# Kernel tuning notes

Hardware: AMD Instinct MI355X
Metric: run time of the kernel (lower is better)

Reference implementation:

```python
import jax, jax.numpy as jnp
import numpy as np

N_NODES = 10000
N_EDGES = 160000
NEG_SLOPE = 0.2


def _gat_layer(x, src, dst, W, a_src, a_dst, bias, concat):
    # x: [N, F_in]; W: [F_in, H*C]; a_src/a_dst: [H, C]; bias: [H*C] or [C]
    N = x.shape[0]
    H, C = a_src.shape
    h = (x @ W).reshape(N, H, C)                       # [N,H,C]
    al_s = jnp.einsum('nhc,hc->nh', h, a_src)          # [N,H]
    al_d = jnp.einsum('nhc,hc->nh', h, a_dst)          # [N,H]
    e = jax.nn.leaky_relu(al_s[src] + al_d[dst], NEG_SLOPE)  # [E,H]
    # segment softmax over incoming edges of each destination node
    m = jax.ops.segment_max(e, dst, num_segments=N)    # [N,H]
    ex = jnp.exp(e - m[dst])
    denom = jax.ops.segment_sum(ex, dst, num_segments=N)
    alpha = ex / (denom[dst] + 1e-16)                  # [E,H]
    msg = h[src] * alpha[:, :, None]                   # [E,H,C]
    out = jax.ops.segment_sum(msg, dst, num_segments=N)  # [N,H,C]
    out = out.reshape(N, H * C) if concat else out.mean(axis=1)
    return out + bias


def setup_inputs() -> dict:
    key = jax.random.key(0)
    ks = jax.random.split(key, 10)
    in_dim, hid, out_dim, heads = 768, 512, 768, 4
    x = jax.random.normal(ks[0], (N_NODES, in_dim), dtype=jnp.float32)
    edge_index = jax.random.randint(ks[1], (2, N_EDGES), 0, N_NODES, dtype=jnp.int64)
    g = lambda k, shape, fan: jax.random.normal(k, shape, jnp.float32) / np.sqrt(fan)
    return {
        'x': x,
        'edge_index': edge_index,
        'W1': g(ks[2], (in_dim, heads * hid), in_dim),
        'att_src1': g(ks[3], (heads, hid), hid),
        'att_dst1': g(ks[4], (heads, hid), hid),
        'b1': jnp.zeros((heads * hid,), jnp.float32),
        'W2': g(ks[5], (heads * hid, out_dim), heads * hid),
        'att_src2': g(ks[6], (1, out_dim), out_dim),
        'att_dst2': g(ks[7], (1, out_dim), out_dim),
        'b2': jnp.zeros((out_dim,), jnp.float32),
    }


def reference(x, edge_index, W1, att_src1, att_dst1, b1, W2, att_src2, att_dst2, b2):
    N = x.shape[0]
    loops = jnp.arange(N, dtype=edge_index.dtype)
    src = jnp.concatenate([edge_index[0], loops])  # PyG GATConv adds self-loops
    dst = jnp.concatenate([edge_index[1], loops])
    h = jax.nn.elu(_gat_layer(x, src, dst, W1, att_src1, att_dst1, b1, concat=True))
    out = _gat_layer(h, src, dst, W2, att_src2, att_dst2, b2, concat=False)
    return out
```

## Files before the change

### kernel.cpp

```cpp
#include <hip/hip_runtime.h>
#include <hip/hip_bf16.h>
#include <math.h>

#define N_NODES 10000
#define N_EDGES0 160000
#define E_TOT (N_EDGES0 + N_NODES)
#define H1 4
#define C1 512
#define F1 2048
#define IN_DIM 768
#define C2 768
#define NEG_SLOPE 0.2f

typedef _Float16 f16x8 __attribute__((ext_vector_type(8)));
typedef _Float16 f16x4 __attribute__((ext_vector_type(4)));
typedef float f32x4 __attribute__((ext_vector_type(4)));

typedef __attribute__((address_space(1))) const void* gas_ptr;
typedef __attribute__((address_space(3))) void* las_ptr;
static __device__ __forceinline__ void gload16(const void* g, void* l) {
  __builtin_amdgcn_global_load_lds((gas_ptr)g, (las_ptr)l, 16, 0, 0);
}

static __device__ __forceinline__ unsigned enc_f(float v) {
  unsigned u = __float_as_uint(v);
  return (u & 0x80000000u) ? ~u : (u | 0x80000000u);
}
static __device__ __forceinline__ float dec_f(unsigned u) {
  return (u & 0x80000000u) ? __uint_as_float(u ^ 0x80000000u)
                           : __uint_as_float(~u);
}

static __device__ __forceinline__ void edge_sd(const int* __restrict__ ei, int e,
                                               int& s, int& d) {
  if (e < N_EDGES0) { s = ei[e]; d = ei[N_EDGES0 + e]; }
  else { s = e - N_EDGES0; d = s; }
}

__global__ void split_k(const float* __restrict__ in, _Float16* __restrict__ hi,
                        _Float16* __restrict__ lo, int n4) {
  int i = blockIdx.x * blockDim.x + threadIdx.x;
  if (i >= n4) return;
  float4 v = ((const float4*)in)[i];
  f16x4 h, l;
  h.x = (_Float16)v.x; l.x = (_Float16)(v.x - (float)h.x);
  h.y = (_Float16)v.y; l.y = (_Float16)(v.y - (float)h.y);
  h.z = (_Float16)v.z; l.z = (_Float16)(v.z - (float)h.z);
  h.w = (_Float16)v.w; l.w = (_Float16)(v.w - (float)h.w);
  ((f16x4*)hi)[i] = h;
  ((f16x4*)lo)[i] = l;
}

__global__ void tsplit_k(const float* __restrict__ W, _Float16* __restrict__ hi,
                         _Float16* __restrict__ lo, int K, int N) {
  __shared__ float tile[32][33];
  const int nb = blockIdx.x * 32, kb = blockIdx.y * 32;
  const int tx = threadIdx.x, ty = threadIdx.y;
  for (int r = ty; r < 32; r += 8)
    tile[r][tx] = W[(size_t)(kb + r) * N + nb + tx];
  __syncthreads();
  for (int r = ty; r < 32; r += 8) {
    float v = tile[tx][r];
    _Float16 h = (_Float16)v;
    hi[(size_t)(nb + r) * K + kb + tx] = h;
    lo[(size_t)(nb + r) * K + kb + tx] = (_Float16)(v - (float)h);
  }
}

__global__ __launch_bounds__(256) void gemm_sf16(
    const _Float16* __restrict__ Ahi, const _Float16* __restrict__ Alo,
    const _Float16* __restrict__ Bhi, const _Float16* __restrict__ Blo,
    float* __restrict__ C, int M, int N, int K) {
  __shared__ _Float16 sAh[128 * 32];
  __shared__ _Float16 sAl[128 * 32];
  __shared__ _Float16 sBh[128 * 32];
  __shared__ _Float16 sBl[128 * 32];

  const int t = threadIdx.x;
  const int w = t >> 6, lane = t & 63;
  const int m0 = blockIdx.y * 128, n0 = blockIdx.x * 128;

  const int o0 = w * 1024 + lane * 16;
  const int o1 = o0 + 4096;
  const int ma0 = o0 >> 6, cb0 = o0 & 63;
  const int ma1 = o1 >> 6, cb1 = o1 & 63;
  const int rA0 = min(m0 + ma0, M - 1), rA1 = min(m0 + ma1, M - 1);
  const size_t gA0 = (size_t)rA0 * K + (cb0 >> 1);
  const size_t gA1 = (size_t)rA1 * K + (cb1 >> 1);
  const size_t gB0 = (size_t)(n0 + ma0) * K + (cb0 >> 1);
  const size_t gB1 = (size_t)(n0 + ma1) * K + (cb1 >> 1);

  char* lA0 = (char*)sAh + w * 1024;
  char* lA1 = lA0 + 4096;
  char* lAl0 = (char*)sAl + w * 1024;
  char* lAl1 = lAl0 + 4096;
  char* lB0 = (char*)sBh + w * 1024;
  char* lB1 = lB0 + 4096;
  char* lBl0 = (char*)sBl + w * 1024;
  char* lBl1 = lBl0 + 4096;

  const int wr = w >> 1, wc = w & 1;
  const int lr = lane & 15, lg = lane >> 4;
  const int aoff = (wr * 64 + lr) * 32 + lg * 8;
  const int boff = (wc * 64 + lr) * 32 + lg * 8;

  f32x4 acc[4][4];
#pragma unroll
  for (int i = 0; i < 4; i++)
#pragma unroll
    for (int j = 0; j < 4; j++) acc[i][j] = (f32x4)(0.f);

  for (int k0 = 0; k0 < K; k0 += 32) {
    __syncthreads();
    gload16(Ahi + gA0 + k0, lA0);
    gload16(Ahi + gA1 + k0, lA1);
    gload16(Alo + gA0 + k0, lAl0);
    gload16(Alo + gA1 + k0, lAl1);
    gload16(Bhi + gB0 + k0, lB0);
    gload16(Bhi + gB1 + k0, lB1);
    gload16(Blo + gB0 + k0, lBl0);
    gload16(Blo + gB1 + k0, lBl1);
    __syncthreads();

    f16x8 ah[4], al[4], bh[4], bl[4];
#pragma unroll
    for (int i = 0; i < 4; i++) {
      ah[i] = *(const f16x8*)&sAh[aoff + i * 16 * 32];
      al[i] = *(const f16x8*)&sAl[aoff + i * 16 * 32];
      bh[i] = *(const f16x8*)&sBh[boff + i * 16 * 32];
      bl[i] = *(const f16x8*)&sBl[boff + i * 16 * 32];
    }
#pragma unroll
    for (int i = 0; i < 4; i++)
#pragma unroll
      for (int j = 0; j < 4; j++) {
        acc[i][j] = __builtin_amdgcn_mfma_f32_16x16x32_f16(ah[i], bh[j], acc[i][j], 0, 0, 0);
        acc[i][j] = __builtin_amdgcn_mfma_f32_16x16x32_f16(ah[i], bl[j], acc[i][j], 0, 0, 0);
        acc[i][j] = __builtin_amdgcn_mfma_f32_16x16x32_f16(al[i], bh[j], acc[i][j], 0, 0, 0);
      }
  }

#pragma unroll
  for (int i = 0; i < 4; i++)
#pragma unroll
    for (int j = 0; j < 4; j++) {
      const int col = n0 + wc * 64 + j * 16 + lr;
      const int rbase = m0 + wr * 64 + i * 16 + lg * 4;
#pragma unroll
      for (int r = 0; r < 4; r++) {
        int row = rbase + r;
        if (row < M) C[(size_t)row * N + col] = acc[i][j][r];
      }
    }
}

__global__ void attn_logits(const float* __restrict__ h,
                            const float* __restrict__ asrc,
                            const float* __restrict__ adst,
                            float* __restrict__ als, float* __restrict__ ald,
                            int NH, int Hh, int C) {
  int w = (blockIdx.x * blockDim.x + threadIdx.x) >> 6;
  int lane = threadIdx.x & 63;
  if (w >= NH) return;
  int hh = w % Hh;
  const float* hp = h + (size_t)w * C;
  const float* sp = asrc + hh * C;
  const float* dp = adst + hh * C;
  float ss = 0.f, sd = 0.f;
  for (int c = lane; c < C; c += 64) {
    float v = hp[c];
    ss = fmaf(v, sp[c], ss);
    sd = fmaf(v, dp[c], sd);
  }
#pragma unroll
  for (int o = 32; o; o >>= 1) {
    ss += __shfl_xor(ss, o);
    sd += __shfl_xor(sd, o);
  }
  if (lane == 0) { als[w] = ss; ald[w] = sd; }
}

__global__ void edge_max_k(const int* __restrict__ ei,
                           const float* __restrict__ als,
                           const float* __restrict__ ald,
                           float* __restrict__ ev, unsigned* __restrict__ menc,
                           int Hh) {
  int idx = blockIdx.x * blockDim.x + threadIdx.x;
  if (idx >= E_TOT * Hh) return;
  int e = idx / Hh, hh = idx - e * Hh;
  int s, d; edge_sd(ei, e, s, d);
  float x = als[s * Hh + hh] + ald[d * Hh + hh];
  float v = x > 0.f ? x : NEG_SLOPE * x;
  ev[idx] = v;
  atomicMax(&menc[d * Hh + hh], enc_f(v));
}

__global__ void edge_exp_k(const int* __restrict__ ei,
                           const unsigned* __restrict__ menc,
                           float* __restrict__ ev, float* __restrict__ denom,
                           int Hh) {
  int idx = blockIdx.x * blockDim.x + threadIdx.x;
  if (idx >= E_TOT * Hh) return;
  int e = idx / Hh, hh = idx - e * Hh;
  int s, d; edge_sd(ei, e, s, d);
  float m = dec_f(menc[d * Hh + hh]);
  float ex = expf(ev[idx] - m);
  ev[idx] = ex;
  atomicAdd(&denom[d * Hh + hh], ex);
}

__global__ void hist_k(const int* __restrict__ ei, int* __restrict__ count) {
  int e = blockIdx.x * blockDim.x + threadIdx.x;
  if (e >= E_TOT) return;
  int s, d; edge_sd(ei, e, s, d);
  atomicAdd(&count[d], 1);
}

__global__ __launch_bounds__(1024) void scan_k(const int* __restrict__ count,
                                               int* __restrict__ rowstart,
                                               int N, int total) {
  __shared__ int sums[1024];
  __shared__ int carry_s;
  int t = threadIdx.x;
  if (t == 0) carry_s = 0;
  __syncthreads();
  for (int base = 0; base < N; base += 1024) {
    int i = base + t;
    int c = (i < N) ? count[i] : 0;
    sums[t] = c;
    __syncthreads();
    for (int off = 1; off < 1024; off <<= 1) {
      int v = (t >= off) ? sums[t - off] : 0;
      __syncthreads();
      sums[t] += v;
      __syncthreads();
    }
    int carry = carry_s;
    if (i < N) rowstart[i] = carry + sums[t] - c;
    __syncthreads();
    if (t == 1023) carry_s = carry + sums[1023];
    __syncthreads();
  }
  if (t == 0) rowstart[N] = total;
}

__global__ void scatter_k(const int* __restrict__ ei,
                          const int* __restrict__ rowstart,
                          int* __restrict__ cursor,
                          int* __restrict__ csr_src, int* __restrict__ csr_eid) {
  int e = blockIdx.x * blockDim.x + threadIdx.x;
  if (e >= E_TOT) return;
  int s, d; edge_sd(ei, e, s, d);
  int pos = rowstart[d] + atomicAdd(&cursor[d], 1);
  csr_src[pos] = s;
  csr_eid[pos] = e;
}

template <int FT, bool ELU, bool SPLIT>
__global__ void aggregate_k(const float* __restrict__ hsrc,
                            const float* __restrict__ ev,
                            const float* __restrict__ denom,
                            const float* __restrict__ bias,
                            const int* __restrict__ rowstart,
                            const int* __restrict__ csr_src,
                            const int* __restrict__ csr_eid,
                            float* __restrict__ out,
                            _Float16* __restrict__ ohi, _Float16* __restrict__ olo,
                            int Hh, int C) {
  const int n = blockIdx.x;
  const int t = threadIdx.x;
  const int F = Hh * C;
  const int f0 = t * FT;
  const int hh = f0 / C;
  const float inv = 1.f / (denom[n * Hh + hh] + 1e-16f);
  float acc[FT];
#pragma unroll
  for (int i = 0; i < FT; i++) acc[i] = 0.f;
  const int j0 = rowstart[n], j1 = rowstart[n + 1];
  for (int j = j0; j < j1; j++) {
    int s = csr_src[j];
    int eid = csr_eid[j];
    float wgt = ev[eid * Hh + hh] * inv;
    const float* hp = hsrc + (size_t)s * F + f0;
#pragma unroll
    for (int i = 0; i < FT; i += 4) {
      float4 v = *(const float4*)(hp + i);
      acc[i]     = fmaf(wgt, v.x, acc[i]);
      acc[i + 1] = fmaf(wgt, v.y, acc[i + 1]);
      acc[i + 2] = fmaf(wgt, v.z, acc[i + 2]);
      acc[i + 3] = fmaf(wgt, v.w, acc[i + 3]);
    }
  }
  if (SPLIT) {
    f16x8 h, l;
#pragma unroll
    for (int i = 0; i < FT; i++) {
      float o = acc[i] + bias[f0 + i];
      if (ELU) o = o > 0.f ? o : expm1f(o);
      _Float16 hv = (_Float16)o;
      h[i & 7] = hv;
      l[i & 7] = (_Float16)(o - (float)hv);
    }
    *(f16x8*)&ohi[(size_t)n * F + f0] = h;
    *(f16x8*)&olo[(size_t)n * F + f0] = l;
  } else {
#pragma unroll
    for (int i = 0; i < FT; i++) {
      float o = acc[i] + bias[f0 + i];
      if (ELU) o = o > 0.f ? o : expm1f(o);
      out[(size_t)n * F + f0 + i] = o;
    }
  }
}

extern "C" void kernel_launch(void* const* d_in, const int* in_sizes, int n_in,
                              void* d_out, int out_size, void* d_ws, size_t ws_size,
                              hipStream_t stream) {
  const float* x   = (const float*)d_in[0];
  const int*   ei  = (const int*)d_in[1];
  const float* W1  = (const float*)d_in[2];
  const float* as1 = (const float*)d_in[3];
  const float* ad1 = (const float*)d_in[4];
  const float* b1  = (const float*)d_in[5];
  const float* W2  = (const float*)d_in[6];
  const float* as2 = (const float*)d_in[7];
  const float* ad2 = (const float*)d_in[8];
  const float* b2  = (const float*)d_in[9];
  float* out = (float*)d_out;

  char* p = (char*)d_ws;
  auto alloc = [&](size_t bytes) {
    char* r = p;
    p += (bytes + 255) & ~(size_t)255;
    return r;
  };
  float*     h1    = (float*)alloc((size_t)N_NODES * F1 * 4);
  _Float16*  xhi   = (_Float16*)alloc((size_t)N_NODES * IN_DIM * 2);
  _Float16*  xlo   = (_Float16*)alloc((size_t)N_NODES * IN_DIM * 2);
  _Float16*  W1hi  = (_Float16*)alloc((size_t)IN_DIM * F1 * 2);
  _Float16*  W1lo  = (_Float16*)alloc((size_t)IN_DIM * F1 * 2);
  _Float16*  W2hi  = (_Float16*)alloc((size_t)F1 * C2 * 2);
  _Float16*  W2lo  = (_Float16*)alloc((size_t)F1 * C2 * 2);
  _Float16*  h2hi  = (_Float16*)alloc((size_t)N_NODES * F1 * 2);
  _Float16*  h2lo  = (_Float16*)alloc((size_t)N_NODES * F1 * 2);
  float*     als   = (float*)alloc((size_t)N_NODES * H1 * 4);
  float*     ald   = (float*)alloc((size_t)N_NODES * H1 * 4);
  unsigned*  menc  = (unsigned*)alloc((size_t)N_NODES * H1 * 4);
  float*     denom = (float*)alloc((size_t)N_NODES * H1 * 4);
  float*     ev    = (float*)alloc((size_t)E_TOT * H1 * 4);
  int*       count    = (int*)alloc((size_t)N_NODES * 4);
  int*       rowstart = (int*)alloc((size_t)(N_NODES + 1) * 4);
  int*       cursor   = (int*)alloc((size_t)N_NODES * 4);
  int*       csr_src  = (int*)alloc((size_t)E_TOT * 4);
  int*       csr_eid  = (int*)alloc((size_t)E_TOT * 4);
  float*     h3 = h1;

  const int EB = (E_TOT + 255) / 256;

  hipMemsetAsync(count, 0, (size_t)N_NODES * 4, stream);
  hipMemsetAsync(cursor, 0, (size_t)N_NODES * 4, stream);
  hist_k<<<EB, 256, 0, stream>>>(ei, count);
  scan_k<<<1, 1024, 0, stream>>>(count, rowstart, N_NODES, E_TOT);
  scatter_k<<<EB, 256, 0, stream>>>(ei, rowstart, cursor, csr_src, csr_eid);

  split_k<<<(N_NODES * IN_DIM / 4 + 255) / 256, 256, 0, stream>>>(x, xhi, xlo,
                                                                  N_NODES * IN_DIM / 4);
  tsplit_k<<<dim3(F1 / 32, IN_DIM / 32), dim3(32, 8), 0, stream>>>(W1, W1hi, W1lo,
                                                                   IN_DIM, F1);
  tsplit_k<<<dim3(C2 / 32, F1 / 32), dim3(32, 8), 0, stream>>>(W2, W2hi, W2lo,
                                                               F1, C2);

  gemm_sf16<<<dim3(F1 / 128, (N_NODES + 127) / 128), 256, 0, stream>>>(
      xhi, xlo, W1hi, W1lo, h1, N_NODES, F1, IN_DIM);
  attn_logits<<<(N_NODES * H1) / 4, 256, 0, stream>>>(h1, as1, ad1, als, ald,
                                                      N_NODES * H1, H1, C1);
  hipMemsetAsync(menc, 0, (size_t)N_NODES * H1 * 4, stream);
  hipMemsetAsync(denom, 0, (size_t)N_NODES * H1 * 4, stream);
  edge_max_k<<<(E_TOT * H1 + 255) / 256, 256, 0, stream>>>(ei, als, ald, ev, menc, H1);
  edge_exp_k<<<(E_TOT * H1 + 255) / 256, 256, 0, stream>>>(ei, menc, ev, denom, H1);
  aggregate_k<8, true, true><<<N_NODES, 256, 0, stream>>>(
      h1, ev, denom, b1, rowstart, csr_src, csr_eid, nullptr, h2hi, h2lo, H1, C1);

  gemm_sf16<<<dim3(C2 / 128, (N_NODES + 127) / 128), 256, 0, stream>>>(
      h2hi, h2lo, W2hi, W2lo, h3, N_NODES, C2, F1);
  attn_logits<<<N_NODES / 4, 256, 0, stream>>>(h3, as2, ad2, als, ald,
                                               N_NODES, 1, C2);
  hipMemsetAsync(menc, 0, (size_t)N_NODES * 4, stream);
  hipMemsetAsync(denom, 0, (size_t)N_NODES * 4, stream);
  edge_max_k<<<EB, 256, 0, stream>>>(ei, als, ald, ev, menc, 1);
  edge_exp_k<<<EB, 256, 0, stream>>>(ei, menc, ev, denom, 1);
  aggregate_k<4, false, false><<<N_NODES, 192, 0, stream>>>(
      h3, ev, denom, b2, rowstart, csr_src, csr_eid, out, nullptr, nullptr, 1, C2);
}
```

Measured before the change: 723.0 us.

## Fuse attention logits into GEMM epilogue and store edge weights in CSR order

The attention-logit dot products move into the GEMM epilogue: each wave reduces its accumulator tile against att_src/att_dst with shuffles and atomically adds partial sums per row and head. This removes the separate attn_logits kernel and its re-read of h. Edge exp values are now written in CSR order through a csr_pos map, so aggregation reads them contiguously without the eid indirection. The aggregation loop is unrolled across several edges to keep more gathers in flight, and the softmax normalization is applied once at the end. In exchange, the GEMM epilogue gains atomics and two extra memsets.

```diff
diff --git a/kernel.cpp b/kernel.cpp
--- a/kernel.cpp
+++ b/kernel.cpp
@@ -70,7 +70,9 @@
 __global__ __launch_bounds__(256) void gemm_sf16(
     const _Float16* __restrict__ Ahi, const _Float16* __restrict__ Alo,
     const _Float16* __restrict__ Bhi, const _Float16* __restrict__ Blo,
-    float* __restrict__ C, int M, int N, int K) {
+    float* __restrict__ C, int M, int N, int K,
+    const float* __restrict__ asrc, const float* __restrict__ adst,
+    float* __restrict__ als, float* __restrict__ ald, int Hh, int Cdim) {
   __shared__ _Float16 sAh[128 * 32];
   __shared__ _Float16 sAl[128 * 32];
   __shared__ _Float16 sBh[128 * 32];
@@ -152,32 +154,38 @@
         if (row < M) C[(size_t)row * N + col] = acc[i][j][r];
       }
     }
-}
-
-__global__ void attn_logits(const float* __restrict__ h,
-                            const float* __restrict__ asrc,
-                            const float* __restrict__ adst,
-                            float* __restrict__ als, float* __restrict__ ald,
-                            int NH, int Hh, int C) {
-  int w = (blockIdx.x * blockDim.x + threadIdx.x) >> 6;
-  int lane = threadIdx.x & 63;
-  if (w >= NH) return;
-  int hh = w % Hh;
-  const float* hp = h + (size_t)w * C;
-  const float* sp = asrc + hh * C;
-  const float* dp = adst + hh * C;
-  float ss = 0.f, sd = 0.f;
-  for (int c = lane; c < C; c += 64) {
-    float v = hp[c];
-    ss = fmaf(v, sp[c], ss);
-    sd = fmaf(v, dp[c], sd);
-  }
-#pragma unroll
-  for (int o = 32; o; o >>= 1) {
-    ss += __shfl_xor(ss, o);
-    sd += __shfl_xor(sd, o);
-  }
-  if (lane == 0) { als[w] = ss; ald[w] = sd; }
+
+  const int head = n0 / Cdim;
+  const int cbase = n0 - head * Cdim + wc * 64 + lr;
+  float asv[4], adv[4];
+#pragma unroll
+  for (int j = 0; j < 4; j++) {
+    asv[j] = asrc[(size_t)head * Cdim + cbase + j * 16];
+    adv[j] = adst[(size_t)head * Cdim + cbase + j * 16];
+  }
+#pragma unroll
+  for (int i = 0; i < 4; i++) {
+    const int rbase = m0 + wr * 64 + i * 16 + lg * 4;
+#pragma unroll
+    for (int r = 0; r < 4; r++) {
+      float ss = 0.f, sd = 0.f;
+#pragma unroll
+      for (int j = 0; j < 4; j++) {
+        float v = acc[i][j][r];
+        ss = fmaf(v, asv[j], ss);
+        sd = fmaf(v, adv[j], sd);
+      }
+#pragma unroll
+      for (int o = 8; o; o >>= 1) {
+        ss += __shfl_xor(ss, o);
+        sd += __shfl_xor(sd, o);
+      }
+      if (lr == 0 && rbase + r < M) {
+        atomicAdd(&als[(size_t)(rbase + r) * Hh + head], ss);
+        atomicAdd(&ald[(size_t)(rbase + r) * Hh + head], sd);
+      }
+    }
+  }
 }
 
 __global__ void edge_max_k(const int* __restrict__ ei,
@@ -197,7 +205,9 @@
 
 __global__ void edge_exp_k(const int* __restrict__ ei,
                            const unsigned* __restrict__ menc,
-                           float* __restrict__ ev, float* __restrict__ denom,
+                           const float* __restrict__ ev,
+                           const int* __restrict__ csr_pos,
+                           float* __restrict__ evs, float* __restrict__ denom,
                            int Hh) {
   int idx = blockIdx.x * blockDim.x + threadIdx.x;
   if (idx >= E_TOT * Hh) return;
@@ -205,7 +215,7 @@
   int s, d; edge_sd(ei, e, s, d);
   float m = dec_f(menc[d * Hh + hh]);
   float ex = expf(ev[idx] - m);
-  ev[idx] = ex;
+  evs[(size_t)csr_pos[e] * Hh + hh] = ex;
   atomicAdd(&denom[d * Hh + hh], ex);
 }
 
@@ -247,26 +257,23 @@
 __global__ void scatter_k(const int* __restrict__ ei,
                           const int* __restrict__ rowstart,
                           int* __restrict__ cursor,
-                          int* __restrict__ csr_src, int* __restrict__ csr_eid) {
+                          int* __restrict__ csr_src, int* __restrict__ csr_pos) {
   int e = blockIdx.x * blockDim.x + threadIdx.x;
   if (e >= E_TOT) return;
   int s, d; edge_sd(ei, e, s, d);
   int pos = rowstart[d] + atomicAdd(&cursor[d], 1);
   csr_src[pos] = s;
-  csr_eid[pos] = e;
+  csr_pos[e] = pos;
 }
 
 template <int FT, bool ELU, bool SPLIT>
-__global__ void aggregate_k(const float* __restrict__ hsrc,
-                            const float* __restrict__ ev,
-                            const float* __restrict__ denom,
-                            const float* __restrict__ bias,
-                            const int* __restrict__ rowstart,
-                            const int* __restrict__ csr_src,
-                            const int* __restrict__ csr_eid,
-                            float* __restrict__ out,
-                            _Float16* __restrict__ ohi, _Float16* __restrict__ olo,
-                            int Hh, int C) {
+__global__ __launch_bounds__(256) void aggregate_k(
+    const float* __restrict__ hsrc, const float* __restrict__ evs,
+    const float* __restrict__ denom, const float* __restrict__ bias,
+    const int* __restrict__ rowstart, const int* __restrict__ csr_src,
+    float* __restrict__ out,
+    _Float16* __restrict__ ohi, _Float16* __restrict__ olo,
+    int Hh, int C) {
   const int n = blockIdx.x;
   const int t = threadIdx.x;
   const int F = Hh * C;
@@ -277,25 +284,52 @@
 #pragma unroll
   for (int i = 0; i < FT; i++) acc[i] = 0.f;
   const int j0 = rowstart[n], j1 = rowstart[n + 1];
-  for (int j = j0; j < j1; j++) {
+
+  constexpr int UN = (FT == 8) ? 4 : 8;
+  int j = j0;
+  for (; j + UN <= j1; j += UN) {
+    int   sidx[UN];
+    float wv[UN];
+#pragma unroll
+    for (int u = 0; u < UN; u++) sidx[u] = csr_src[j + u];
+#pragma unroll
+    for (int u = 0; u < UN; u++) wv[u] = evs[(size_t)(j + u) * Hh + hh];
+    float4 va[UN][FT / 4];
+#pragma unroll
+    for (int u = 0; u < UN; u++) {
+      const float* hp = hsrc + (size_t)sidx[u] * F + f0;
+#pragma unroll
+      for (int q = 0; q < FT / 4; q++) va[u][q] = *(const float4*)(hp + q * 4);
+    }
+#pragma unroll
+    for (int u = 0; u < UN; u++)
+#pragma unroll
+      for (int q = 0; q < FT / 4; q++) {
+        acc[q * 4 + 0] = fmaf(wv[u], va[u][q].x, acc[q * 4 + 0]);
+        acc[q * 4 + 1] = fmaf(wv[u], va[u][q].y, acc[q * 4 + 1]);
+        acc[q * 4 + 2] = fmaf(wv[u], va[u][q].z, acc[q * 4 + 2]);
+        acc[q * 4 + 3] = fmaf(wv[u], va[u][q].w, acc[q * 4 + 3]);
+      }
+  }
+  for (; j < j1; j++) {
     int s = csr_src[j];
-    int eid = csr_eid[j];
-    float wgt = ev[eid * Hh + hh] * inv;
+    float wgt = evs[(size_t)j * Hh + hh];
     const float* hp = hsrc + (size_t)s * F + f0;
 #pragma unroll
-    for (int i = 0; i < FT; i += 4) {
-      float4 v = *(const float4*)(hp + i);
-      acc[i]     = fmaf(wgt, v.x, acc[i]);
-      acc[i + 1] = fmaf(wgt, v.y, acc[i + 1]);
-      acc[i + 2] = fmaf(wgt, v.z, acc[i + 2]);
-      acc[i + 3] = fmaf(wgt, v.w, acc[i + 3]);
-    }
-  }
+    for (int q = 0; q < FT / 4; q++) {
+      float4 v = *(const float4*)(hp + q * 4);
+      acc[q * 4 + 0] = fmaf(wgt, v.x, acc[q * 4 + 0]);
+      acc[q * 4 + 1] = fmaf(wgt, v.y, acc[q * 4 + 1]);
+      acc[q * 4 + 2] = fmaf(wgt, v.z, acc[q * 4 + 2]);
+      acc[q * 4 + 3] = fmaf(wgt, v.w, acc[q * 4 + 3]);
+    }
+  }
+
   if (SPLIT) {
     f16x8 h, l;
 #pragma unroll
     for (int i = 0; i < FT; i++) {
-      float o = acc[i] + bias[f0 + i];
+      float o = acc[i] * inv + bias[f0 + i];
       if (ELU) o = o > 0.f ? o : expm1f(o);
       _Float16 hv = (_Float16)o;
       h[i & 7] = hv;
@@ -306,7 +340,7 @@
   } else {
 #pragma unroll
     for (int i = 0; i < FT; i++) {
-      float o = acc[i] + bias[f0 + i];
+      float o = acc[i] * inv + bias[f0 + i];
       if (ELU) o = o > 0.f ? o : expm1f(o);
       out[(size_t)n * F + f0 + i] = o;
     }
@@ -348,11 +382,12 @@
   unsigned*  menc  = (unsigned*)alloc((size_t)N_NODES * H1 * 4);
   float*     denom = (float*)alloc((size_t)N_NODES * H1 * 4);
   float*     ev    = (float*)alloc((size_t)E_TOT * H1 * 4);
+  float*     evs   = (float*)alloc((size_t)E_TOT * H1 * 4);
   int*       count    = (int*)alloc((size_t)N_NODES * 4);
   int*       rowstart = (int*)alloc((size_t)(N_NODES + 1) * 4);
   int*       cursor   = (int*)alloc((size_t)N_NODES * 4);
   int*       csr_src  = (int*)alloc((size_t)E_TOT * 4);
-  int*       csr_eid  = (int*)alloc((size_t)E_TOT * 4);
+  int*       csr_pos  = (int*)alloc((size_t)E_TOT * 4);
   float*     h3 = h1;
 
   const int EB = (E_TOT + 255) / 256;
@@ -361,7 +396,7 @@
   hipMemsetAsync(cursor, 0, (size_t)N_NODES * 4, stream);
   hist_k<<<EB, 256, 0, stream>>>(ei, count);
   scan_k<<<1, 1024, 0, stream>>>(count, rowstart, N_NODES, E_TOT);
-  scatter_k<<<EB, 256, 0, stream>>>(ei, rowstart, cursor, csr_src, csr_eid);
+  scatter_k<<<EB, 256, 0, stream>>>(ei, rowstart, cursor, csr_src, csr_pos);
 
   split_k<<<(N_NODES * IN_DIM / 4 + 255) / 256, 256, 0, stream>>>(x, xhi, xlo,
                                                                   N_NODES * IN_DIM / 4);
@@ -370,25 +405,28 @@
   tsplit_k<<<dim3(C2 / 32, F1 / 32), dim3(32, 8), 0, stream>>>(W2, W2hi, W2lo,
                                                                F1, C2);
 
+  hipMemsetAsync(als, 0, (size_t)N_NODES * H1 * 4, stream);
+  hipMemsetAsync(ald, 0, (size_t)N_NODES * H1 * 4, stream);
   gemm_sf16<<<dim3(F1 / 128, (N_NODES + 127) / 128), 256, 0, stream>>>(
-      xhi, xlo, W1hi, W1lo, h1, N_NODES, F1, IN_DIM);
-  attn_logits<<<(N_NODES * H1) / 4, 256, 0, stream>>>(h1, as1, ad1, als, ald,
-                                                      N_NODES * H1, H1, C1);
+      xhi, xlo, W1hi, W1lo, h1, N_NODES, F1, IN_DIM,
+      as1, ad1, als, ald, H1, C1);
   hipMemsetAsync(menc, 0, (size_t)N_NODES * H1 * 4, stream);
   hipMemsetAsync(denom, 0, (size_t)N_NODES * H1 * 4, stream);
   edge_max_k<<<(E_TOT * H1 + 255) / 256, 256, 0, stream>>>(ei, als, ald, ev, menc, H1);
-  edge_exp_k<<<(E_TOT * H1 + 255) / 256, 256, 0, stream>>>(ei, menc, ev, denom, H1);
+  edge_exp_k<<<(E_TOT * H1 + 255) / 256, 256, 0, stream>>>(ei, menc, ev, csr_pos,
+                                                           evs, denom, H1);
   aggregate_k<8, true, true><<<N_NODES, 256, 0, stream>>>(
-      h1, ev, denom, b1, rowstart, csr_src, csr_eid, nullptr, h2hi, h2lo, H1, C1);
-
+      h1, evs, denom, b1, rowstart, csr_src, nullptr, h2hi, h2lo, H1, C1);
+
+  hipMemsetAsync(als, 0, (size_t)N_NODES * 4, stream);
+  hipMemsetAsync(ald, 0, (size_t)N_NODES * 4, stream);
   gemm_sf16<<<dim3(C2 / 128, (N_NODES + 127) / 128), 256, 0, stream>>>(
-      h2hi, h2lo, W2hi, W2lo, h3, N_NODES, C2, F1);
-  attn_logits<<<N_NODES / 4, 256, 0, stream>>>(h3, as2, ad2, als, ald,
-                                               N_NODES, 1, C2);
+      h2hi, h2lo, W2hi, W2lo, h3, N_NODES, C2, F1,
+      as2, ad2, als, ald, 1, C2);
   hipMemsetAsync(menc, 0, (size_t)N_NODES * 4, stream);
   hipMemsetAsync(denom, 0, (size_t)N_NODES * 4, stream);
   edge_max_k<<<EB, 256, 0, stream>>>(ei, als, ald, ev, menc, 1);
-  edge_exp_k<<<EB, 256, 0, stream>>>(ei, menc, ev, denom, 1);
+  edge_exp_k<<<EB, 256, 0, stream>>>(ei, menc, ev, csr_pos, evs, denom, 1);
   aggregate_k<4, false, false><<<N_NODES, 192, 0, stream>>>(
-      h3, ev, denom, b2, rowstart, csr_src, csr_eid, out, nullptr, nullptr, 1, C2);
-}
+      h3, evs, denom, b2, rowstart, csr_src, out, nullptr, nullptr, 1, C2);
+}
```

After: 737.6 us. +2.0%, slower.
